# Optimization experiments

Measured on AMD Instinct MI355X. Metric: run time of the kernel, lower is better.

Reference implementation:

```python
import jax, jax.numpy as jnp
import numpy as np

TEMPERATURE = 0.1
EPS = 1e-8


def setup_inputs() -> dict:
    key = jax.random.key(0)
    k1, k2 = jax.random.split(key)
    N, D = 4096, 256
    z_i = jax.random.normal(k1, (N, D), dtype=jnp.float32)
    z_j = jax.random.normal(k2, (N, D), dtype=jnp.float32)
    return {"z_i": z_i, "z_j": z_j}


def reference(z_i, z_j):
    N = z_i.shape[0]
    zi = z_i.reshape(N, -1)
    zj = z_j.reshape(N, -1)
    z = jnp.concatenate([zi, zj], axis=0)  # [2N, D]
    # cosine similarity: normalize rows once, then a single GEMM
    norms = jnp.linalg.norm(z, axis=1, keepdims=True)
    zn = z / jnp.maximum(norms, EPS)
    sim = zn @ zn.T  # [2N, 2N]
    idx = jnp.arange(N)
    sim_ij = sim[idx, idx + N]   # diag offset +N
    sim_ji = sim[idx + N, idx]   # diag offset -N
    positives = jnp.concatenate([sim_ij, sim_ji], axis=0)  # [2N]
    # denominator: row-mean of exp(sim / t) over all 2N columns (incl. self)
    denom_mean = jnp.mean(jnp.exp(sim / TEMPERATURE), axis=1)  # [2N]
    all_losses = -(positives / TEMPERATURE - jnp.log(denom_mean))
    loss = jnp.sum(all_losses) / (2 * N)
    return loss
```

## Files before the change

### kernel.cpp

```cpp
#include <hip/hip_runtime.h>
#include <hip/hip_bf16.h>
#include <math.h>

#define NN 4096
#define DD 256
#define TWO_N 8192
#define SCALE 14.426950408889634f
#define INV_2N (1.0f/8192.0f)

typedef __bf16 bf16_t;
typedef bf16_t bf16x8 __attribute__((ext_vector_type(8)));
typedef bf16_t bf16x4 __attribute__((ext_vector_type(4)));
typedef float f32x4 __attribute__((ext_vector_type(4)));

__global__ __launch_bounds__(256) void knorm(const float* __restrict__ zi,
                                             const float* __restrict__ zj,
                                             bf16_t* __restrict__ zn) {
    const int wid = threadIdx.x >> 6, lane = threadIdx.x & 63;
    const int row = blockIdx.x * 4 + wid;
    const float* src = (row < NN) ? (zi + (size_t)row * DD)
                                  : (zj + (size_t)(row - NN) * DD);
    float4 v = *(const float4*)(src + lane * 4);
    float ss = v.x*v.x + v.y*v.y + v.z*v.z + v.w*v.w;
    #pragma unroll
    for (int m = 1; m < 64; m <<= 1) ss += __shfl_xor(ss, m);
    const float sc = 1.0f / fmaxf(sqrtf(ss), 1e-8f);
    bf16x4 o;
    o[0] = (bf16_t)(v.x * sc);
    o[1] = (bf16_t)(v.y * sc);
    o[2] = (bf16_t)(v.z * sc);
    o[3] = (bf16_t)(v.w * sc);
    *(bf16x4*)(zn + (size_t)row * DD + lane * 4) = o;
}

__global__ __launch_bounds__(512, 2) void kmain(const bf16_t* __restrict__ zn,
                                                float* __restrict__ partial) {
    __shared__ char lds[2][8192];
    const int tid = threadIdx.x, wid = tid >> 6, lane = tid & 63;
    const int rb = blockIdx.x >> 4, cs = blockIdx.x & 15;
    const int rowbase = rb * 512 + wid * 64;
    const int colbase = cs * 512;
    const int ar = lane & 15, ak = lane >> 4;

    bf16x8 afrag[4][8];
    #pragma unroll
    for (int s = 0; s < 4; ++s)
        #pragma unroll
        for (int kk = 0; kk < 8; ++kk)
            afrag[s][kk] = *(const bf16x8*)(zn + (size_t)(rowbase + s*16 + ar) * DD
                                            + kk*32 + ak*8);

    float racc[4][4];
    #pragma unroll
    for (int s = 0; s < 4; ++s)
        #pragma unroll
        for (int j = 0; j < 4; ++j) racc[s][j] = 0.0f;

    const char* gz = (const char*)zn;

    auto stage = [&](int buf, int ct) {
        const int dd  = wid * 1024 + lane * 16;
        const int src = dd ^ (((dd >> 9) & 7) << 4);
        const char* gp = gz + (size_t)(colbase + ct * 16) * 512 + src;
        __builtin_amdgcn_global_load_lds(
            (const __attribute__((address_space(1))) void*)gp,
            (__attribute__((address_space(3))) void*)(&lds[buf][wid * 1024]),
            16, 0, 0);
    };

    stage(0, 0);

    const int brow  = lane & 15;
    const int bcol0 = (lane >> 4) * 16;
    const int bxor  = (brow & 7) << 4;
    const int baddr = brow * 512;

    for (int ct = 0; ct < 32; ++ct) {
        const int cur = ct & 1;
        __syncthreads();
        if (ct + 1 < 32) stage(cur ^ 1, ct + 1);

        f32x4 c0 = {0,0,0,0}, c1 = {0,0,0,0}, c2 = {0,0,0,0}, c3 = {0,0,0,0};
        #pragma unroll
        for (int kk = 0; kk < 8; ++kk) {
            const int a = baddr + ((kk * 64 + bcol0) ^ bxor);
            bf16x8 b = *(const bf16x8*)(&lds[cur][a]);
            c0 = __builtin_amdgcn_mfma_f32_16x16x32_bf16(afrag[0][kk], b, c0, 0, 0, 0);
            c1 = __builtin_amdgcn_mfma_f32_16x16x32_bf16(afrag[1][kk], b, c1, 0, 0, 0);
            c2 = __builtin_amdgcn_mfma_f32_16x16x32_bf16(afrag[2][kk], b, c2, 0, 0, 0);
            c3 = __builtin_amdgcn_mfma_f32_16x16x32_bf16(afrag[3][kk], b, c3, 0, 0, 0);
        }
        #pragma unroll
        for (int j = 0; j < 4; ++j) {
            racc[0][j] += __builtin_amdgcn_exp2f(c0[j] * SCALE);
            racc[1][j] += __builtin_amdgcn_exp2f(c1[j] * SCALE);
            racc[2][j] += __builtin_amdgcn_exp2f(c2[j] * SCALE);
            racc[3][j] += __builtin_amdgcn_exp2f(c3[j] * SCALE);
        }
        __syncthreads();
    }

    #pragma unroll
    for (int s = 0; s < 4; ++s)
        #pragma unroll
        for (int j = 0; j < 4; ++j) {
            float v = racc[s][j];
            v += __shfl_xor(v, 1); v += __shfl_xor(v, 2);
            v += __shfl_xor(v, 4); v += __shfl_xor(v, 8);
            if ((lane & 15) == 0)
                partial[cs * TWO_N + rowbase + s*16 + (lane >> 4)*4 + j] = v;
        }
}

__global__ __launch_bounds__(256) void kfinal(const bf16_t* __restrict__ zn,
                                              const float* __restrict__ partial,
                                              float* __restrict__ out) {
    __shared__ float red[4];
    const int wid = threadIdx.x >> 6, lane = threadIdx.x & 63;
    const int gw = blockIdx.x * 4 + wid;
    float acc = 0.0f;
    for (int it = 0; it < 16; ++it) {
        const int i = gw + it * 256;
        const bf16_t* pa = zn + (size_t)i * DD;
        const bf16_t* pb = zn + (size_t)(i + NN) * DD;
        bf16x4 av = *(const bf16x4*)(pa + lane * 4);
        bf16x4 bv = *(const bf16x4*)(pb + lane * 4);
        float d = 0.0f;
        #pragma unroll
        for (int j = 0; j < 4; ++j) d += (float)av[j] * (float)bv[j];
        #pragma unroll
        for (int m = 1; m < 64; m <<= 1) d += __shfl_xor(d, m);
        float ri = 0.0f, rj = 0.0f;
        if (lane < 16) {
            ri = partial[lane * TWO_N + i];
            rj = partial[lane * TWO_N + i + NN];
        }
        #pragma unroll
        for (int m = 1; m < 16; m <<= 1) { ri += __shfl_xor(ri, m); rj += __shfl_xor(rj, m); }
        if (lane == 0)
            acc += logf(ri * INV_2N) + logf(rj * INV_2N) - 20.0f * d;
    }
    if (lane == 0) red[wid] = acc;
    __syncthreads();
    if (threadIdx.x == 0) {
        atomicAdd(out, (red[0] + red[1] + red[2] + red[3]) * INV_2N);
    }
}

extern "C" void kernel_launch(void* const* d_in, const int* in_sizes, int n_in,
                              void* d_out, int out_size, void* d_ws, size_t ws_size,
                              hipStream_t stream) {
    const float* zi = (const float*)d_in[0];
    const float* zj = (const float*)d_in[1];
    bf16_t* zn      = (bf16_t*)d_ws;
    float*  partial = (float*)((char*)d_ws + (size_t)TWO_N * DD * 2);
    float*  out     = (float*)d_out;

    hipMemsetAsync(d_out, 0, sizeof(float), stream);
    knorm <<<TWO_N / 4, 256, 0, stream>>>(zi, zj, zn);
    kmain <<<256, 512, 0, stream>>>(zn, partial);
    kfinal<<<64, 256, 0, stream>>>(zn, partial, out);
}
```

Before: 115.6 us.

## Exploit similarity matrix symmetry with upper-triangular tiles and atomic row sums

The main kernel now computes only the upper-triangular 128x128 tiles of the symmetric similarity matrix (2080 blocks). Each tile's exp-sums are credited to both its row and column indices through atomics, so roughly half the GEMM and exp work is removed. Positives are taken from the accumulator diagonal of the offset tiles instead of being recomputed in the final kernel. The output memset is folded into the normalization kernel. In exchange there are many float atomics, the K loop is no longer software-pipelined, and block-index decoding uses a serial loop.

```diff
diff --git a/kernel.cpp b/kernel.cpp
--- a/kernel.cpp
+++ b/kernel.cpp
@@ -15,9 +15,18 @@
 
 __global__ __launch_bounds__(256) void knorm(const float* __restrict__ zi,
                                              const float* __restrict__ zj,
-                                             bf16_t* __restrict__ zn) {
+                                             bf16_t* __restrict__ zn,
+                                             float* __restrict__ rowsum,
+                                             float* __restrict__ possum,
+                                             float* __restrict__ out) {
     const int wid = threadIdx.x >> 6, lane = threadIdx.x & 63;
-    const int row = blockIdx.x * 4 + wid;
+    const int b = blockIdx.x;
+    if (b < 8) {
+        f32x4 z = {0, 0, 0, 0};
+        *(f32x4*)(rowsum + b * 1024 + threadIdx.x * 4) = z;
+        if (b == 0 && threadIdx.x == 0) { possum[0] = 0.0f; out[0] = 0.0f; }
+    }
+    const int row = b * 4 + wid;
     const float* src = (row < NN) ? (zi + (size_t)row * DD)
                                   : (zj + (size_t)(row - NN) * DD);
     float4 v = *(const float4*)(src + lane * 4);
@@ -33,117 +42,129 @@
     *(bf16x4*)(zn + (size_t)row * DD + lane * 4) = o;
 }
 
-__global__ __launch_bounds__(512, 2) void kmain(const bf16_t* __restrict__ zn,
-                                                float* __restrict__ partial) {
-    __shared__ char lds[2][8192];
+__global__ __launch_bounds__(256, 4) void kmain(const bf16_t* __restrict__ zn,
+                                                float* __restrict__ rowsum,
+                                                float* __restrict__ possum) {
+    __shared__ char ldsA[16384];
+    __shared__ char ldsB[16384];
     const int tid = threadIdx.x, wid = tid >> 6, lane = tid & 63;
-    const int rb = blockIdx.x >> 4, cs = blockIdx.x & 15;
-    const int rowbase = rb * 512 + wid * 64;
-    const int colbase = cs * 512;
-    const int ar = lane & 15, ak = lane >> 4;
 
-    bf16x8 afrag[4][8];
+    int ti = 0, rem = blockIdx.x;
+    while (rem >= 64 - ti) { rem -= 64 - ti; ++ti; }
+    const int tj = ti + rem;
+    const int rowbase = ti << 7, colbase = tj << 7;
+
+    const int wr = wid >> 1, wc = wid & 1;
+    const int lo = lane & 15, hi = lane >> 4;
+
+    f32x4 acc[4][4];
     #pragma unroll
     for (int s = 0; s < 4; ++s)
         #pragma unroll
-        for (int kk = 0; kk < 8; ++kk)
-            afrag[s][kk] = *(const bf16x8*)(zn + (size_t)(rowbase + s*16 + ar) * DD
-                                            + kk*32 + ak*8);
-
-    float racc[4][4];
-    #pragma unroll
-    for (int s = 0; s < 4; ++s)
-        #pragma unroll
-        for (int j = 0; j < 4; ++j) racc[s][j] = 0.0f;
+        for (int t = 0; t < 4; ++t) acc[s][t] = (f32x4){0, 0, 0, 0};
 
     const char* gz = (const char*)zn;
 
-    auto stage = [&](int buf, int ct) {
-        const int dd  = wid * 1024 + lane * 16;
-        const int src = dd ^ (((dd >> 9) & 7) << 4);
-        const char* gp = gz + (size_t)(colbase + ct * 16) * 512 + src;
-        __builtin_amdgcn_global_load_lds(
-            (const __attribute__((address_space(1))) void*)gp,
-            (__attribute__((address_space(3))) void*)(&lds[buf][wid * 1024]),
-            16, 0, 0);
-    };
+    for (int ks = 0; ks < 4; ++ks) {
+        #pragma unroll
+        for (int p = 0; p < 4; ++p) {
+            const int base = p * 4096 + wid * 1024;
+            const int dd   = base + lane * 16;
+            const int row  = dd >> 7, col = dd & 127;
+            const int scol = col ^ ((row & 7) << 4);
+            const char* ga = gz + (size_t)(rowbase + row) * 512 + ks * 128 + scol;
+            const char* gb = gz + (size_t)(colbase + row) * 512 + ks * 128 + scol;
+            __builtin_amdgcn_global_load_lds(
+                (const __attribute__((address_space(1))) void*)ga,
+                (__attribute__((address_space(3))) void*)(&ldsA[base]), 16, 0, 0);
+            __builtin_amdgcn_global_load_lds(
+                (const __attribute__((address_space(1))) void*)gb,
+                (__attribute__((address_space(3))) void*)(&ldsB[base]), 16, 0, 0);
+        }
+        __syncthreads();
 
-    stage(0, 0);
+        #pragma unroll
+        for (int kk = 0; kk < 2; ++kk) {
+            bf16x8 af[4], bfr[4];
+            const int kb = kk * 64 + hi * 16;
+            const int sw = kb ^ ((lo & 7) << 4);
+            #pragma unroll
+            for (int s = 0; s < 4; ++s) {
+                af[s]  = *(const bf16x8*)(&ldsA[(wr * 64 + s * 16 + lo) * 128 + sw]);
+                bfr[s] = *(const bf16x8*)(&ldsB[(wc * 64 + s * 16 + lo) * 128 + sw]);
+            }
+            #pragma unroll
+            for (int s = 0; s < 4; ++s)
+                #pragma unroll
+                for (int t = 0; t < 4; ++t)
+                    acc[s][t] = __builtin_amdgcn_mfma_f32_16x16x32_bf16(
+                        af[s], bfr[t], acc[s][t], 0, 0, 0);
+        }
+        __syncthreads();
+    }
 
-    const int brow  = lane & 15;
-    const int bcol0 = (lane >> 4) * 16;
-    const int bxor  = (brow & 7) << 4;
-    const int baddr = brow * 512;
-
-    for (int ct = 0; ct < 32; ++ct) {
-        const int cur = ct & 1;
-        __syncthreads();
-        if (ct + 1 < 32) stage(cur ^ 1, ct + 1);
-
-        f32x4 c0 = {0,0,0,0}, c1 = {0,0,0,0}, c2 = {0,0,0,0}, c3 = {0,0,0,0};
-        #pragma unroll
-        for (int kk = 0; kk < 8; ++kk) {
-            const int a = baddr + ((kk * 64 + bcol0) ^ bxor);
-            bf16x8 b = *(const bf16x8*)(&lds[cur][a]);
-            c0 = __builtin_amdgcn_mfma_f32_16x16x32_bf16(afrag[0][kk], b, c0, 0, 0, 0);
-            c1 = __builtin_amdgcn_mfma_f32_16x16x32_bf16(afrag[1][kk], b, c1, 0, 0, 0);
-            c2 = __builtin_amdgcn_mfma_f32_16x16x32_bf16(afrag[2][kk], b, c2, 0, 0, 0);
-            c3 = __builtin_amdgcn_mfma_f32_16x16x32_bf16(afrag[3][kk], b, c3, 0, 0, 0);
+    if (tj == ti + 32 && wr == wc) {
+        const int j = lo - hi * 4;
+        float p = 0.0f;
+        if (j >= 0 && j < 4) {
+            #pragma unroll
+            for (int s = 0; s < 4; ++s) p += acc[s][s][j];
         }
         #pragma unroll
-        for (int j = 0; j < 4; ++j) {
-            racc[0][j] += __builtin_amdgcn_exp2f(c0[j] * SCALE);
-            racc[1][j] += __builtin_amdgcn_exp2f(c1[j] * SCALE);
-            racc[2][j] += __builtin_amdgcn_exp2f(c2[j] * SCALE);
-            racc[3][j] += __builtin_amdgcn_exp2f(c3[j] * SCALE);
-        }
-        __syncthreads();
+        for (int m = 1; m < 64; m <<= 1) p += __shfl_xor(p, m);
+        if (lane == 0) atomicAdd(possum, p);
     }
 
     #pragma unroll
     for (int s = 0; s < 4; ++s)
         #pragma unroll
+        for (int t = 0; t < 4; ++t)
+            #pragma unroll
+            for (int j = 0; j < 4; ++j)
+                acc[s][t][j] = __builtin_amdgcn_exp2f(acc[s][t][j] * SCALE);
+
+    #pragma unroll
+    for (int s = 0; s < 4; ++s) {
+        f32x4 rs = acc[s][0] + acc[s][1] + acc[s][2] + acc[s][3];
+        #pragma unroll
         for (int j = 0; j < 4; ++j) {
-            float v = racc[s][j];
+            float v = rs[j];
             v += __shfl_xor(v, 1); v += __shfl_xor(v, 2);
             v += __shfl_xor(v, 4); v += __shfl_xor(v, 8);
-            if ((lane & 15) == 0)
-                partial[cs * TWO_N + rowbase + s*16 + (lane >> 4)*4 + j] = v;
+            if (lo == 0)
+                atomicAdd(&rowsum[rowbase + wr * 64 + s * 16 + hi * 4 + j], v);
         }
+    }
+
+    if (ti != tj) {
+        #pragma unroll
+        for (int t = 0; t < 4; ++t) {
+            float v = 0.0f;
+            #pragma unroll
+            for (int s = 0; s < 4; ++s)
+                v += acc[s][t][0] + acc[s][t][1] + acc[s][t][2] + acc[s][t][3];
+            v += __shfl_xor(v, 16); v += __shfl_xor(v, 32);
+            if (hi == 0)
+                atomicAdd(&rowsum[colbase + wc * 64 + t * 16 + lo], v);
+        }
+    }
 }
 
-__global__ __launch_bounds__(256) void kfinal(const bf16_t* __restrict__ zn,
-                                              const float* __restrict__ partial,
+__global__ __launch_bounds__(256) void kfinal(const float* __restrict__ rowsum,
+                                              const float* __restrict__ possum,
                                               float* __restrict__ out) {
     __shared__ float red[4];
     const int wid = threadIdx.x >> 6, lane = threadIdx.x & 63;
-    const int gw = blockIdx.x * 4 + wid;
-    float acc = 0.0f;
-    for (int it = 0; it < 16; ++it) {
-        const int i = gw + it * 256;
-        const bf16_t* pa = zn + (size_t)i * DD;
-        const bf16_t* pb = zn + (size_t)(i + NN) * DD;
-        bf16x4 av = *(const bf16x4*)(pa + lane * 4);
-        bf16x4 bv = *(const bf16x4*)(pb + lane * 4);
-        float d = 0.0f;
-        #pragma unroll
-        for (int j = 0; j < 4; ++j) d += (float)av[j] * (float)bv[j];
-        #pragma unroll
-        for (int m = 1; m < 64; m <<= 1) d += __shfl_xor(d, m);
-        float ri = 0.0f, rj = 0.0f;
-        if (lane < 16) {
-            ri = partial[lane * TWO_N + i];
-            rj = partial[lane * TWO_N + i + NN];
-        }
-        #pragma unroll
-        for (int m = 1; m < 16; m <<= 1) { ri += __shfl_xor(ri, m); rj += __shfl_xor(rj, m); }
-        if (lane == 0)
-            acc += logf(ri * INV_2N) + logf(rj * INV_2N) - 20.0f * d;
-    }
-    if (lane == 0) red[wid] = acc;
+    const int gid = blockIdx.x * 256 + threadIdx.x;
+    float v = logf(rowsum[gid] * INV_2N);
+    #pragma unroll
+    for (int m = 1; m < 64; m <<= 1) v += __shfl_xor(v, m);
+    if (lane == 0) red[wid] = v;
     __syncthreads();
     if (threadIdx.x == 0) {
-        atomicAdd(out, (red[0] + red[1] + red[2] + red[3]) * INV_2N);
+        float s = red[0] + red[1] + red[2] + red[3];
+        if (blockIdx.x == 0) s -= 20.0f * possum[0];
+        atomicAdd(out, s * INV_2N);
     }
 }
 
@@ -152,12 +173,12 @@
                               hipStream_t stream) {
     const float* zi = (const float*)d_in[0];
     const float* zj = (const float*)d_in[1];
-    bf16_t* zn      = (bf16_t*)d_ws;
-    float*  partial = (float*)((char*)d_ws + (size_t)TWO_N * DD * 2);
-    float*  out     = (float*)d_out;
+    bf16_t* zn     = (bf16_t*)d_ws;
+    float*  rowsum = (float*)((char*)d_ws + (size_t)TWO_N * DD * 2);
+    float*  possum = rowsum + TWO_N;
+    float*  out    = (float*)d_out;
 
-    hipMemsetAsync(d_out, 0, sizeof(float), stream);
-    knorm <<<TWO_N / 4, 256, 0, stream>>>(zi, zj, zn);
-    kmain <<<256, 512, 0, stream>>>(zn, partial);
-    kfinal<<<64, 256, 0, stream>>>(zn, partial, out);
+    knorm <<<2048, 256, 0, stream>>>(zi, zj, zn, rowsum, possum, out);
+    kmain <<<2080, 256, 0, stream>>>(zn, rowsum, possum);
+    kfinal<<<32,   256, 0, stream>>>(rowsum, possum, out);
 }
```

Measured after the change: 103.1 us. -10.8%, faster.
